# Kernel optimization log

Measured on AMD Instinct MI355X. Metric: run time of the kernel, lower is better.

Reference implementation:

```python
import jax, jax.numpy as jnp
import numpy as np

N_HEADS = 8
EMBED_DIM = 512
HEAD_DIM = EMBED_DIM // N_HEADS
INPUT_DIM = 512


def setup_inputs() -> dict:
    key = jax.random.key(0)
    ks = jax.random.split(key, 9)
    B, N = 4, 2048
    s_in = 1.0 / np.sqrt(INPUT_DIM)
    s_e = 1.0 / np.sqrt(EMBED_DIM)
    return {
        "q": jax.random.normal(ks[0], (B, N, INPUT_DIM), dtype=jnp.float32),
        "wq": jax.random.uniform(ks[1], (EMBED_DIM, INPUT_DIM), jnp.float32, -s_in, s_in),
        "bq": jax.random.uniform(ks[2], (EMBED_DIM,), jnp.float32, -s_in, s_in),
        "wk": jax.random.uniform(ks[3], (EMBED_DIM, INPUT_DIM), jnp.float32, -s_in, s_in),
        "bk": jax.random.uniform(ks[4], (EMBED_DIM,), jnp.float32, -s_in, s_in),
        "wv": jax.random.uniform(ks[5], (EMBED_DIM, INPUT_DIM), jnp.float32, -s_in, s_in),
        "bv": jax.random.uniform(ks[6], (EMBED_DIM,), jnp.float32, -s_in, s_in),
        "wo": jax.random.uniform(ks[7], (EMBED_DIM, EMBED_DIM), jnp.float32, -s_e, s_e),
        "bo": jax.random.uniform(ks[8], (EMBED_DIM,), jnp.float32, -s_e, s_e),
    }


def reference(q, wq, bq, wk, bk, wv, bv, wo, bo):
    B, N, _ = q.shape
    # linear projections (torch Linear: x @ W.T + b)
    Q = (q @ wq.T + bq).reshape(B, N, N_HEADS, HEAD_DIM).transpose(0, 2, 1, 3)
    K = (q @ wk.T + bk).reshape(B, N, N_HEADS, HEAD_DIM).transpose(0, 2, 1, 3)
    V = (q @ wv.T + bv).reshape(B, N, N_HEADS, HEAD_DIM).transpose(0, 2, 1, 3)
    scores = jnp.einsum("bhqd,bhkd->bhqk", Q, K) / jnp.sqrt(
        jnp.asarray(HEAD_DIM, dtype=q.dtype)
    )
    weights = jax.nn.softmax(scores, axis=-1)
    out = jnp.einsum("bhqk,bhkd->bhqd", weights, V)  # [B,H,N,Dh]
    out = out.transpose(0, 2, 1, 3).reshape(B, N, EMBED_DIM)
    return out @ wo.T + bo
```

## Files before the change

### kernel.cpp

```cpp
#include <hip/hip_runtime.h>
#include <hip/hip_bf16.h>
#include <math.h>

#define SEQ    2048
#define DH     64
#define EMB    512
#define INDIM  512
#define NHEADS 8
#define BATCH  4
#define MTOT   (BATCH * SEQ)

typedef __attribute__((ext_vector_type(8))) short bf16x8;
typedef __attribute__((ext_vector_type(4))) float f32x4;

__device__ __forceinline__ ushort f2bf(float x) {
  union { float f; unsigned u; } v; v.f = x;
  unsigned r = v.u + 0x7FFFu + ((v.u >> 16) & 1u);
  return (ushort)(r >> 16);
}

__device__ __forceinline__ unsigned cvt_pk_bf16(float lo, float hi) {
  unsigned r;
  asm("v_cvt_pk_bf16_f32 %0, %1, %2" : "=v"(r) : "v"(lo), "v"(hi));
  return r;
}

__device__ __forceinline__ float fast_exp2(float x) {
  float r;
  asm("v_exp_f32 %0, %1" : "=v"(r) : "v"(x));
  return r;
}

__device__ __forceinline__ void permswap32(unsigned &x, unsigned &y) {
  asm("v_permlane32_swap_b32 %0, %1" : "+v"(x), "+v"(y));
}

__global__ __launch_bounds__(256) void conv_bf16(const float* __restrict__ src,
                                                 ushort* __restrict__ dst, int n8) {
  const int i = blockIdx.x * 256 + threadIdx.x;
  if (i >= n8) return;
  const float4 a = ((const float4*)src)[i * 2];
  const float4 b = ((const float4*)src)[i * 2 + 1];
  uint4 o;
  o.x = cvt_pk_bf16(a.x, a.y);
  o.y = cvt_pk_bf16(a.z, a.w);
  o.z = cvt_pk_bf16(b.x, b.y);
  o.w = cvt_pk_bf16(b.z, b.w);
  ((uint4*)dst)[i] = o;
}

__global__ __launch_bounds__(256) void conv_bf16_w4(
    const float* __restrict__ w0, const float* __restrict__ w1,
    const float* __restrict__ w2, const float* __restrict__ w3,
    ushort* __restrict__ dst, int n8per) {
  const int i = blockIdx.x * 256 + threadIdx.x;
  if (i >= n8per) return;
  const float* src = (blockIdx.y == 0) ? w0 : (blockIdx.y == 1) ? w1
                   : (blockIdx.y == 2) ? w2 : w3;
  ushort* d = dst + (size_t)blockIdx.y * n8per * 8;
  const float4 a = ((const float4*)src)[i * 2];
  const float4 b = ((const float4*)src)[i * 2 + 1];
  uint4 o;
  o.x = cvt_pk_bf16(a.x, a.y);
  o.y = cvt_pk_bf16(a.z, a.w);
  o.z = cvt_pk_bf16(b.x, b.y);
  o.w = cvt_pk_bf16(b.z, b.w);
  ((uint4*)d)[i] = o;
}

template <int MODE>
__global__ __launch_bounds__(256) void mfma_gemm(
    const ushort* __restrict__ A, const ushort* __restrict__ W,
    const float* __restrict__ b0, const float* __restrict__ b1,
    const float* __restrict__ b2,
    ushort* __restrict__ outQ, ushort* __restrict__ outK,
    ushort* __restrict__ outVT, float* __restrict__ outF) {
  constexpr int BM = (MODE == 0) ? 128 : 64;
  constexpr int MF = (MODE == 0) ? 4 : 2;
  __shared__ __align__(16) char smem[MODE == 0 ? 35840 : 12288];
  ushort* As = (ushort*)smem;
  ushort* Bs = (ushort*)(smem + (MODE == 0 ? 8192 : 4096));
  ushort* Tl = (ushort*)smem;
  ushort* Tl2 = (ushort*)smem;

  const int bm = blockIdx.x * BM;
  const int bn = blockIdx.y * 128;
  const int tid = threadIdx.x;
  const int wave = tid >> 6, lane = tid & 63;
  const int g = lane >> 4, ln = lane & 15;
  const int wr = wave >> 1, wc = wave & 1;

  f32x4 acc[MF][4];
#pragma unroll
  for (int m = 0; m < MF; ++m)
#pragma unroll
    for (int n = 0; n < 4; ++n) acc[m][n] = (f32x4){0.f, 0.f, 0.f, 0.f};

  const size_t a_base = (size_t)(bm + wave * 16 + (lane >> 2)) * INDIM + (lane & 3) * 8;
  const size_t b_base = (size_t)(bn + wave * 16 + (lane >> 2)) * INDIM + (lane & 3) * 8;
  ushort* ldsA0 = As + wave * 512;
  ushort* ldsA1 = As + 2048 + wave * 512;
  ushort* ldsB0 = Bs + wave * 512;
  ushort* ldsB1 = Bs + 2048 + wave * 512;

  for (int k0 = 0; k0 < INDIM; k0 += 32) {
    __syncthreads();
    __builtin_amdgcn_global_load_lds(
        (const __attribute__((address_space(1))) void*)(A + a_base + k0),
        (__attribute__((address_space(3))) void*)ldsA0, 16, 0, 0);
    if (MODE == 0)
      __builtin_amdgcn_global_load_lds(
          (const __attribute__((address_space(1))) void*)(A + a_base + 64 * INDIM + k0),
          (__attribute__((address_space(3))) void*)ldsA1, 16, 0, 0);
    __builtin_amdgcn_global_load_lds(
        (const __attribute__((address_space(1))) void*)(W + b_base + k0),
        (__attribute__((address_space(3))) void*)ldsB0, 16, 0, 0);
    __builtin_amdgcn_global_load_lds(
        (const __attribute__((address_space(1))) void*)(W + b_base + 64 * INDIM + k0),
        (__attribute__((address_space(3))) void*)ldsB1, 16, 0, 0);
    __syncthreads();

    bf16x8 af[MF], bfv[4];
#pragma unroll
    for (int m = 0; m < MF; ++m)
      af[m] = *(const bf16x8*)&As[((MODE == 0 ? 64 : 32) * wr + 16 * m + ln) * 32 + 8 * g];
#pragma unroll
    for (int n = 0; n < 4; ++n)
      bfv[n] = *(const bf16x8*)&Bs[(64 * wc + 16 * n + ln) * 32 + 8 * g];
#pragma unroll
    for (int m = 0; m < MF; ++m)
#pragma unroll
      for (int n = 0; n < 4; ++n)
        acc[m][n] = __builtin_amdgcn_mfma_f32_16x16x32_bf16(af[m], bfv[n], acc[m][n], 0, 0, 0);
  }

  if (MODE == 1) {
#pragma unroll
    for (int n = 0; n < 4; ++n) {
      const int e = bn + 64 * wc + 16 * n + ln;
      const float bv = b0[e];
#pragma unroll
      for (int m = 0; m < MF; ++m)
#pragma unroll
        for (int r = 0; r < 4; ++r) {
          const int row = bm + 32 * wr + 16 * m + 4 * g + r;
          outF[(size_t)row * EMB + e] = acc[m][n][r] + bv;
        }
    }
    return;
  }

  const int which = bn >> 9;
  const float* bias = (which == 0) ? b0 : (which == 1) ? b1 : b2;

  if (which < 2) {
    const float scl = (which == 0) ? 0.18033688f : 1.0f;
    ushort* dst = (which == 0) ? outQ : outK;
    __syncthreads();
#pragma unroll
    for (int n = 0; n < 4; ++n) {
      const int cl = 64 * wc + 16 * n + ln;
      const float bv = bias[(bn & 511) + cl];
#pragma unroll
      for (int m = 0; m < 4; ++m)
#pragma unroll
        for (int r = 0; r < 4; ++r) {
          const int rl = 64 * wr + 16 * m + 4 * g + r;
          Tl2[rl * 136 + cl] = f2bf((acc[m][n][r] + bv) * scl);
        }
    }
    __syncthreads();
#pragma unroll
    for (int j = 0; j < 8; ++j) {
      const int cid = j * 256 + tid;
      const int seg = cid >> 3;
      const int l8 = cid & 7;
      const int rl = seg >> 1, half = seg & 1;
      const int row = bm + rl;
      const int b = row >> 11, nn = row & (SEQ - 1);
      const int h = ((bn & 511) >> 6) + half;
      const bf16x8 v = *(const bf16x8*)&Tl2[rl * 136 + half * 64 + l8 * 8];
      *(bf16x8*)&dst[(((size_t)(b * NHEADS + h) * SEQ) + nn) * DH + l8 * 8] = v;
    }
  } else {
    __syncthreads();
#pragma unroll
    for (int n = 0; n < 4; ++n) {
      const int cl = 64 * wc + 16 * n + ln;
      const float bv = bias[(bn & 511) + cl];
#pragma unroll
      for (int m = 0; m < 4; ++m)
#pragma unroll
        for (int r = 0; r < 4; ++r) {
          const int rl = 64 * wr + 16 * m + 4 * g + r;
          Tl[cl * 140 + rl] = f2bf(acc[m][n][r] + bv);
        }
    }
    __syncthreads();
    const int c = tid >> 1;
    const int rh = (tid & 1) * 64;
    const int e = (bn & 511) + c;
    const int h = e >> 6, d = e & 63;
    const int b = bm >> 11;
    const int nn0 = (bm & (SEQ - 1)) + rh;
    ushort* drow = outVT + (((size_t)(b * NHEADS + h) * DH) + d) * SEQ + nn0;
#pragma unroll
    for (int j = 0; j < 8; ++j)
      *(bf16x8*)&drow[j * 8] = *(const bf16x8*)&Tl[c * 140 + rh + j * 8];
  }
}

__global__ __launch_bounds__(256) void attn_mfma(const ushort* __restrict__ Q,
                                                 const ushort* __restrict__ K,
                                                 const ushort* __restrict__ VT,
                                                 ushort* __restrict__ O) {
  __shared__ __align__(16) ushort Kl[2][128 * 72];
  __shared__ __align__(16) ushort Vl[2][64 * 136];

  const int tid = threadIdx.x;
  const int wave = tid >> 6, lane = tid & 63;
  const int g = lane >> 4, ln = lane & 15;

  const int orig = blockIdx.x;
  const int swz = (orig & 7) * 64 + (orig >> 3);
  const int bh = swz >> 4;
  const int qx = swz & 15;
  const int qbase = qx * 128 + wave * 32;

  const ushort* Qb = Q + ((size_t)bh * SEQ + qbase) * DH;
  const ushort* Kb = K + (size_t)bh * SEQ * DH;
  const ushort* Vb = VT + (size_t)bh * DH * SEQ;

  const bf16x8 qfA0 = *(const bf16x8*)&Qb[ln * DH + 8 * g];
  const bf16x8 qfA1 = *(const bf16x8*)&Qb[ln * DH + 32 + 8 * g];
  const bf16x8 qfB0 = *(const bf16x8*)&Qb[(16 + ln) * DH + 8 * g];
  const bf16x8 qfB1 = *(const bf16x8*)&Qb[(16 + ln) * DH + 32 + 8 * g];

  bf16x8 vones;
#pragma unroll
  for (int i = 0; i < 8; ++i) vones[i] = (short)0x3F80;

  f32x4 oaccA[4], oaccB[4];
  f32x4 oaccDA = (f32x4){0.f, 0.f, 0.f, 0.f};
  f32x4 oaccDB = (f32x4){0.f, 0.f, 0.f, 0.f};
#pragma unroll
  for (int t = 0; t < 4; ++t) {
    oaccA[t] = (f32x4){0.f, 0.f, 0.f, 0.f};
    oaccB[t] = (f32x4){0.f, 0.f, 0.f, 0.f};
  }

  const int skv = tid >> 3, sd = (tid & 7) * 8;
  const int dt = tid >> 2, kc = (tid & 3) * 8;
  int pr[4];
#pragma unroll
  for (int j = 0; j < 4; ++j) {
    const int row = skv + 32 * j;
    pr[j] = row ^ (((((row >> 2) ^ (row >> 3)) & 1)) * 12);
  }

  bf16x8 kv[4], vv[4];
#pragma unroll
  for (int j = 0; j < 4; ++j) {
    kv[j] = *(const bf16x8*)&Kb[(size_t)(skv + 32 * j) * DH + sd];
    vv[j] = *(const bf16x8*)&Vb[(size_t)dt * SEQ + kc + 32 * j];
  }
#pragma unroll
  for (int j = 0; j < 4; ++j) {
    *(bf16x8*)&Kl[0][pr[j] * 72 + sd] = kv[j];
    *(bf16x8*)&Vl[0][dt * 136 + kc + 32 * j] = vv[j];
  }
#pragma unroll
  for (int j = 0; j < 4; ++j) {
    kv[j] = *(const bf16x8*)&Kb[(size_t)(128 + skv + 32 * j) * DH + sd];
    vv[j] = *(const bf16x8*)&Vb[(size_t)dt * SEQ + 128 + kc + 32 * j];
  }
  asm volatile("s_waitcnt lgkmcnt(0)" ::: "memory");
  __builtin_amdgcn_s_barrier();

  for (int it = 0; it < 16; ++it) {
    const int cur = it & 1;
    const ushort* Kc = Kl[cur];
    const ushort* Vc = Vl[cur];

    if (it < 15) {
      ushort* Kn = Kl[cur ^ 1];
      ushort* Vn = Vl[cur ^ 1];
#pragma unroll
      for (int j = 0; j < 4; ++j) {
        *(bf16x8*)&Kn[pr[j] * 72 + sd] = kv[j];
        *(bf16x8*)&Vn[dt * 136 + kc + 32 * j] = vv[j];
      }
    }
    {
      const int nxt = (it + 2 < 16) ? (it + 2) * 128 : 15 * 128;
#pragma unroll
      for (int j = 0; j < 4; ++j) {
        kv[j] = *(const bf16x8*)&Kb[(size_t)(nxt + skv + 32 * j) * DH + sd];
        vv[j] = *(const bf16x8*)&Vb[(size_t)dt * SEQ + nxt + kc + 32 * j];
      }
    }

#pragma unroll
    for (int s = 0; s < 2; ++s) {
      bf16x8 ka[4][2], vb[2][4];
#pragma unroll
      for (int t = 0; t < 4; ++t) {
        ka[t][0] = *(const bf16x8*)&Kc[(64 * s + 16 * t + ln) * 72 + 8 * g];
        ka[t][1] = *(const bf16x8*)&Kc[(64 * s + 16 * t + ln) * 72 + 32 + 8 * g];
      }
#pragma unroll
      for (int c = 0; c < 2; ++c)
#pragma unroll
        for (int t = 0; t < 4; ++t)
          vb[c][t] = *(const bf16x8*)&Vc[(16 * t + ln) * 136 + 64 * s + 32 * c + 8 * g];

      f32x4 sA0 = (f32x4){0.f, 0.f, 0.f, 0.f};
      f32x4 sA1 = sA0, sA2 = sA0, sA3 = sA0;
      f32x4 sB0 = sA0, sB1 = sA0, sB2 = sA0, sB3 = sA0;
      __builtin_amdgcn_s_setprio(1);
      sA0 = __builtin_amdgcn_mfma_f32_16x16x32_bf16(ka[0][0], qfA0, sA0, 0, 0, 0);
      sB0 = __builtin_amdgcn_mfma_f32_16x16x32_bf16(ka[0][0], qfB0, sB0, 0, 0, 0);
      sA1 = __builtin_amdgcn_mfma_f32_16x16x32_bf16(ka[1][0], qfA0, sA1, 0, 0, 0);
      sB1 = __builtin_amdgcn_mfma_f32_16x16x32_bf16(ka[1][0], qfB0, sB1, 0, 0, 0);
      sA2 = __builtin_amdgcn_mfma_f32_16x16x32_bf16(ka[2][0], qfA0, sA2, 0, 0, 0);
      sB2 = __builtin_amdgcn_mfma_f32_16x16x32_bf16(ka[2][0], qfB0, sB2, 0, 0, 0);
      sA3 = __builtin_amdgcn_mfma_f32_16x16x32_bf16(ka[3][0], qfA0, sA3, 0, 0, 0);
      sB3 = __builtin_amdgcn_mfma_f32_16x16x32_bf16(ka[3][0], qfB0, sB3, 0, 0, 0);
      sA0 = __builtin_amdgcn_mfma_f32_16x16x32_bf16(ka[0][1], qfA1, sA0, 0, 0, 0);
      sB0 = __builtin_amdgcn_mfma_f32_16x16x32_bf16(ka[0][1], qfB1, sB0, 0, 0, 0);
      sA1 = __builtin_amdgcn_mfma_f32_16x16x32_bf16(ka[1][1], qfA1, sA1, 0, 0, 0);
      sB1 = __builtin_amdgcn_mfma_f32_16x16x32_bf16(ka[1][1], qfB1, sB1, 0, 0, 0);
      sA2 = __builtin_amdgcn_mfma_f32_16x16x32_bf16(ka[2][1], qfA1, sA2, 0, 0, 0);
      sB2 = __builtin_amdgcn_mfma_f32_16x16x32_bf16(ka[2][1], qfB1, sB2, 0, 0, 0);
      sA3 = __builtin_amdgcn_mfma_f32_16x16x32_bf16(ka[3][1], qfA1, sA3, 0, 0, 0);
      sB3 = __builtin_amdgcn_mfma_f32_16x16x32_bf16(ka[3][1], qfB1, sB3, 0, 0, 0);
      __builtin_amdgcn_s_setprio(0);

      float pA0[4], pA1[4], pA2[4], pA3[4];
      float pB0[4], pB1[4], pB2[4], pB3[4];
#pragma unroll
      for (int r = 0; r < 4; ++r) {
        pA0[r] = fast_exp2(sA0[r]);
        pA1[r] = fast_exp2(sA1[r]);
        pA2[r] = fast_exp2(sA2[r]);
        pA3[r] = fast_exp2(sA3[r]);
        pB0[r] = fast_exp2(sB0[r]);
        pB1[r] = fast_exp2(sB1[r]);
        pB2[r] = fast_exp2(sB2[r]);
        pB3[r] = fast_exp2(sB3[r]);
      }

      unsigned aa0 = cvt_pk_bf16(pA0[0], pA0[1]);
      unsigned aa2 = cvt_pk_bf16(pA1[0], pA1[1]);
      unsigned aa1 = cvt_pk_bf16(pA0[2], pA0[3]);
      unsigned aa3 = cvt_pk_bf16(pA1[2], pA1[3]);
      permswap32(aa0, aa2);
      permswap32(aa1, aa3);
      unsigned ab0 = cvt_pk_bf16(pA2[0], pA2[1]);
      unsigned ab2 = cvt_pk_bf16(pA3[0], pA3[1]);
      unsigned ab1 = cvt_pk_bf16(pA2[2], pA2[3]);
      unsigned ab3 = cvt_pk_bf16(pA3[2], pA3[3]);
      permswap32(ab0, ab2);
      permswap32(ab1, ab3);
      unsigned ba0 = cvt_pk_bf16(pB0[0], pB0[1]);
      unsigned ba2 = cvt_pk_bf16(pB1[0], pB1[1]);
      unsigned ba1 = cvt_pk_bf16(pB0[2], pB0[3]);
      unsigned ba3 = cvt_pk_bf16(pB1[2], pB1[3]);
      permswap32(ba0, ba2);
      permswap32(ba1, ba3);
      unsigned bb0 = cvt_pk_bf16(pB2[0], pB2[1]);
      unsigned bb2 = cvt_pk_bf16(pB3[0], pB3[1]);
      unsigned bb1 = cvt_pk_bf16(pB2[2], pB2[3]);
      unsigned bb3 = cvt_pk_bf16(pB3[2], pB3[3]);
      permswap32(bb0, bb2);
      permswap32(bb1, bb3);
      union { unsigned u[4]; bf16x8 v; } paA0, paA1, paB0, paB1;
      paA0.u[0] = aa0; paA0.u[1] = aa1; paA0.u[2] = aa2; paA0.u[3] = aa3;
      paA1.u[0] = ab0; paA1.u[1] = ab1; paA1.u[2] = ab2; paA1.u[3] = ab3;
      paB0.u[0] = ba0; paB0.u[1] = ba1; paB0.u[2] = ba2; paB0.u[3] = ba3;
      paB1.u[0] = bb0; paB1.u[1] = bb1; paB1.u[2] = bb2; paB1.u[3] = bb3;

      __builtin_amdgcn_s_setprio(1);
#pragma unroll
      for (int t = 0; t < 4; ++t) {
        oaccA[t] = __builtin_amdgcn_mfma_f32_16x16x32_bf16(paA0.v, vb[0][t], oaccA[t], 0, 0, 0);
        oaccB[t] = __builtin_amdgcn_mfma_f32_16x16x32_bf16(paB0.v, vb[0][t], oaccB[t], 0, 0, 0);
        oaccA[t] = __builtin_amdgcn_mfma_f32_16x16x32_bf16(paA1.v, vb[1][t], oaccA[t], 0, 0, 0);
        oaccB[t] = __builtin_amdgcn_mfma_f32_16x16x32_bf16(paB1.v, vb[1][t], oaccB[t], 0, 0, 0);
      }
      oaccDA = __builtin_amdgcn_mfma_f32_16x16x32_bf16(paA0.v, vones, oaccDA, 0, 0, 0);
      oaccDB = __builtin_amdgcn_mfma_f32_16x16x32_bf16(paB0.v, vones, oaccDB, 0, 0, 0);
      oaccDA = __builtin_amdgcn_mfma_f32_16x16x32_bf16(paA1.v, vones, oaccDA, 0, 0, 0);
      oaccDB = __builtin_amdgcn_mfma_f32_16x16x32_bf16(paB1.v, vones, oaccDB, 0, 0, 0);
      __builtin_amdgcn_s_setprio(0);
    }

    asm volatile("s_waitcnt lgkmcnt(0)" ::: "memory");
    __builtin_amdgcn_s_barrier();
  }

  const int b = bh >> 3, h = bh & 7;
#pragma unroll
  for (int r = 0; r < 4; ++r) {
    const float irA = 1.0f / oaccDA[r];
    const float irB = 1.0f / oaccDB[r];
    ushort* opA = O + ((size_t)(b * SEQ) + qbase + 4 * g + r) * EMB + h * 64;
    ushort* opB = O + ((size_t)(b * SEQ) + qbase + 16 + 4 * g + r) * EMB + h * 64;
#pragma unroll
    for (int t = 0; t < 4; ++t) {
      opA[16 * t + ln] = f2bf(oaccA[t][r] * irA);
      opB[16 * t + ln] = f2bf(oaccB[t][r] * irB);
    }
  }
}

extern "C" void kernel_launch(void* const* d_in, const int* in_sizes, int n_in,
                              void* d_out, int out_size, void* d_ws, size_t ws_size,
                              hipStream_t stream) {
  const float* q  = (const float*)d_in[0];
  const float* wq = (const float*)d_in[1];
  const float* bq = (const float*)d_in[2];
  const float* wk = (const float*)d_in[3];
  const float* bk = (const float*)d_in[4];
  const float* wv = (const float*)d_in[5];
  const float* bv = (const float*)d_in[6];
  const float* wo = (const float*)d_in[7];
  const float* bo = (const float*)d_in[8];
  float* out = (float*)d_out;

  const size_t XSZ = (size_t)MTOT * INDIM;
  const size_t WSZ = (size_t)EMB * INDIM;
  const size_t QSZ = (size_t)BATCH * NHEADS * SEQ * DH;
  ushort* wsX = (ushort*)d_ws;
  ushort* wsW = wsX + XSZ;
  ushort* wsQ = wsW + 4 * WSZ;
  ushort* wsK = wsQ + QSZ;
  ushort* wsVT = wsK + QSZ;
  ushort* wsA = wsVT + QSZ;

  const dim3 blk(256);

  conv_bf16<<<dim3(XSZ / 8 / 256), blk, 0, stream>>>(q, wsX, XSZ / 8);
  conv_bf16_w4<<<dim3(WSZ / 8 / 256, 4), blk, 0, stream>>>(wq, wk, wv, wo, wsW, WSZ / 8);

  mfma_gemm<0><<<dim3(MTOT / 128, 1536 / 128), blk, 0, stream>>>(
      wsX, wsW, bq, bk, bv, wsQ, wsK, wsVT, nullptr);

  attn_mfma<<<dim3(512), blk, 0, stream>>>(wsQ, wsK, wsVT, wsA);

  mfma_gemm<1><<<dim3(MTOT / 64, EMB / 128), blk, 0, stream>>>(
      wsA, wsW + 3 * WSZ, bo, nullptr, nullptr, nullptr, nullptr, nullptr, out);
}
```

Baseline: 98.89 us.

## Split attention KV range across two thread halves and merge partial accumulators

The attention kernel now runs 512 threads per block. Each 256-thread half processes one half of the key/value sequence (1024 keys) for the same 128 queries, using 64-key tiles per iteration. The halves merge their partial output and denominator accumulators through shared memory at the end. This is split-K inside a block, meant to double the waves in flight per block and raise latency hiding and occupancy with only 512 blocks. The cost is an extra LDS reduction, smaller tiles per barrier, and a launch-bound that may constrain registers. The merge is exact only because the softmax uses no running max, which the kernel already did before.

```diff
diff --git a/kernel.cpp b/kernel.cpp
--- a/kernel.cpp
+++ b/kernel.cpp
@@ -210,15 +210,17 @@
   }
 }
 
-__global__ __launch_bounds__(256) void attn_mfma(const ushort* __restrict__ Q,
-                                                 const ushort* __restrict__ K,
-                                                 const ushort* __restrict__ VT,
-                                                 ushort* __restrict__ O) {
-  __shared__ __align__(16) ushort Kl[2][128 * 72];
-  __shared__ __align__(16) ushort Vl[2][64 * 136];
+__global__ __launch_bounds__(512, 4) void attn_mfma(const ushort* __restrict__ Q,
+                                                    const ushort* __restrict__ K,
+                                                    const ushort* __restrict__ VT,
+                                                    ushort* __restrict__ O) {
+  __shared__ __align__(16) ushort Kl[2][2][64 * 72];
+  __shared__ __align__(16) ushort Vl[2][2][64 * 72];
 
   const int tid = threadIdx.x;
-  const int wave = tid >> 6, lane = tid & 63;
+  const int half = tid >> 8;
+  const int ltid = tid & 255;
+  const int wave = ltid >> 6, lane = ltid & 63;
   const int g = lane >> 4, ln = lane & 15;
 
   const int orig = blockIdx.x;
@@ -226,6 +228,7 @@
   const int bh = swz >> 4;
   const int qx = swz & 15;
   const int qbase = qx * 128 + wave * 32;
+  const int kvbase = half << 10;
 
   const ushort* Qb = Q + ((size_t)bh * SEQ + qbase) * DH;
   const ushort* Kb = K + (size_t)bh * SEQ * DH;
@@ -249,167 +252,179 @@
     oaccB[t] = (f32x4){0.f, 0.f, 0.f, 0.f};
   }
 
-  const int skv = tid >> 3, sd = (tid & 7) * 8;
-  const int dt = tid >> 2, kc = (tid & 3) * 8;
-  int pr[4];
-#pragma unroll
-  for (int j = 0; j < 4; ++j) {
-    const int row = skv + 32 * j;
-    pr[j] = row ^ (((((row >> 2) ^ (row >> 3)) & 1)) * 12);
-  }
-
-  bf16x8 kv[4], vv[4];
-#pragma unroll
-  for (int j = 0; j < 4; ++j) {
-    kv[j] = *(const bf16x8*)&Kb[(size_t)(skv + 32 * j) * DH + sd];
-    vv[j] = *(const bf16x8*)&Vb[(size_t)dt * SEQ + kc + 32 * j];
-  }
-#pragma unroll
-  for (int j = 0; j < 4; ++j) {
-    *(bf16x8*)&Kl[0][pr[j] * 72 + sd] = kv[j];
-    *(bf16x8*)&Vl[0][dt * 136 + kc + 32 * j] = vv[j];
-  }
-#pragma unroll
-  for (int j = 0; j < 4; ++j) {
-    kv[j] = *(const bf16x8*)&Kb[(size_t)(128 + skv + 32 * j) * DH + sd];
-    vv[j] = *(const bf16x8*)&Vb[(size_t)dt * SEQ + 128 + kc + 32 * j];
-  }
+  const int skv = ltid >> 3, sd = (ltid & 7) * 8;
+  const int dt = ltid >> 2, kc = (ltid & 3) * 8;
+  const int pr0 = skv ^ (((((skv >> 2) ^ (skv >> 3)) & 1)) * 12);
+  const int s32 = skv + 32;
+  const int pr1 = s32 ^ (((((s32 >> 2) ^ (s32 >> 3)) & 1)) * 12);
+
+  bf16x8 k0v = *(const bf16x8*)&Kb[(size_t)(kvbase + skv) * DH + sd];
+  bf16x8 k1v = *(const bf16x8*)&Kb[(size_t)(kvbase + 32 + skv) * DH + sd];
+  bf16x8 v0v = *(const bf16x8*)&Vb[(size_t)dt * SEQ + kvbase + kc];
+  bf16x8 v1v = *(const bf16x8*)&Vb[(size_t)dt * SEQ + kvbase + 32 + kc];
+  *(bf16x8*)&Kl[half][0][pr0 * 72 + sd] = k0v;
+  *(bf16x8*)&Kl[half][0][pr1 * 72 + sd] = k1v;
+  *(bf16x8*)&Vl[half][0][dt * 72 + kc] = v0v;
+  *(bf16x8*)&Vl[half][0][dt * 72 + 32 + kc] = v1v;
+  k0v = *(const bf16x8*)&Kb[(size_t)(kvbase + 64 + skv) * DH + sd];
+  k1v = *(const bf16x8*)&Kb[(size_t)(kvbase + 96 + skv) * DH + sd];
+  v0v = *(const bf16x8*)&Vb[(size_t)dt * SEQ + kvbase + 64 + kc];
+  v1v = *(const bf16x8*)&Vb[(size_t)dt * SEQ + kvbase + 96 + kc];
   asm volatile("s_waitcnt lgkmcnt(0)" ::: "memory");
   __builtin_amdgcn_s_barrier();
 
   for (int it = 0; it < 16; ++it) {
     const int cur = it & 1;
-    const ushort* Kc = Kl[cur];
-    const ushort* Vc = Vl[cur];
+    const ushort* Kc = Kl[half][cur];
+    const ushort* Vc = Vl[half][cur];
 
     if (it < 15) {
-      ushort* Kn = Kl[cur ^ 1];
-      ushort* Vn = Vl[cur ^ 1];
-#pragma unroll
-      for (int j = 0; j < 4; ++j) {
-        *(bf16x8*)&Kn[pr[j] * 72 + sd] = kv[j];
-        *(bf16x8*)&Vn[dt * 136 + kc + 32 * j] = vv[j];
-      }
+      ushort* Kn = Kl[half][cur ^ 1];
+      ushort* Vn = Vl[half][cur ^ 1];
+      *(bf16x8*)&Kn[pr0 * 72 + sd] = k0v;
+      *(bf16x8*)&Kn[pr1 * 72 + sd] = k1v;
+      *(bf16x8*)&Vn[dt * 72 + kc] = v0v;
+      *(bf16x8*)&Vn[dt * 72 + 32 + kc] = v1v;
     }
     {
-      const int nxt = (it + 2 < 16) ? (it + 2) * 128 : 15 * 128;
-#pragma unroll
-      for (int j = 0; j < 4; ++j) {
-        kv[j] = *(const bf16x8*)&Kb[(size_t)(nxt + skv + 32 * j) * DH + sd];
-        vv[j] = *(const bf16x8*)&Vb[(size_t)dt * SEQ + nxt + kc + 32 * j];
-      }
-    }
-
-#pragma unroll
-    for (int s = 0; s < 2; ++s) {
-      bf16x8 ka[4][2], vb[2][4];
-#pragma unroll
-      for (int t = 0; t < 4; ++t) {
-        ka[t][0] = *(const bf16x8*)&Kc[(64 * s + 16 * t + ln) * 72 + 8 * g];
-        ka[t][1] = *(const bf16x8*)&Kc[(64 * s + 16 * t + ln) * 72 + 32 + 8 * g];
-      }
-#pragma unroll
-      for (int c = 0; c < 2; ++c)
-#pragma unroll
-        for (int t = 0; t < 4; ++t)
-          vb[c][t] = *(const bf16x8*)&Vc[(16 * t + ln) * 136 + 64 * s + 32 * c + 8 * g];
-
-      f32x4 sA0 = (f32x4){0.f, 0.f, 0.f, 0.f};
-      f32x4 sA1 = sA0, sA2 = sA0, sA3 = sA0;
-      f32x4 sB0 = sA0, sB1 = sA0, sB2 = sA0, sB3 = sA0;
-      __builtin_amdgcn_s_setprio(1);
-      sA0 = __builtin_amdgcn_mfma_f32_16x16x32_bf16(ka[0][0], qfA0, sA0, 0, 0, 0);
-      sB0 = __builtin_amdgcn_mfma_f32_16x16x32_bf16(ka[0][0], qfB0, sB0, 0, 0, 0);
-      sA1 = __builtin_amdgcn_mfma_f32_16x16x32_bf16(ka[1][0], qfA0, sA1, 0, 0, 0);
-      sB1 = __builtin_amdgcn_mfma_f32_16x16x32_bf16(ka[1][0], qfB0, sB1, 0, 0, 0);
-      sA2 = __builtin_amdgcn_mfma_f32_16x16x32_bf16(ka[2][0], qfA0, sA2, 0, 0, 0);
-      sB2 = __builtin_amdgcn_mfma_f32_16x16x32_bf16(ka[2][0], qfB0, sB2, 0, 0, 0);
-      sA3 = __builtin_amdgcn_mfma_f32_16x16x32_bf16(ka[3][0], qfA0, sA3, 0, 0, 0);
-      sB3 = __builtin_amdgcn_mfma_f32_16x16x32_bf16(ka[3][0], qfB0, sB3, 0, 0, 0);
-      sA0 = __builtin_amdgcn_mfma_f32_16x16x32_bf16(ka[0][1], qfA1, sA0, 0, 0, 0);
-      sB0 = __builtin_amdgcn_mfma_f32_16x16x32_bf16(ka[0][1], qfB1, sB0, 0, 0, 0);
-      sA1 = __builtin_amdgcn_mfma_f32_16x16x32_bf16(ka[1][1], qfA1, sA1, 0, 0, 0);
-      sB1 = __builtin_amdgcn_mfma_f32_16x16x32_bf16(ka[1][1], qfB1, sB1, 0, 0, 0);
-      sA2 = __builtin_amdgcn_mfma_f32_16x16x32_bf16(ka[2][1], qfA1, sA2, 0, 0, 0);
-      sB2 = __builtin_amdgcn_mfma_f32_16x16x32_bf16(ka[2][1], qfB1, sB2, 0, 0, 0);
-      sA3 = __builtin_amdgcn_mfma_f32_16x16x32_bf16(ka[3][1], qfA1, sA3, 0, 0, 0);
-      sB3 = __builtin_amdgcn_mfma_f32_16x16x32_bf16(ka[3][1], qfB1, sB3, 0, 0, 0);
-      __builtin_amdgcn_s_setprio(0);
-
-      float pA0[4], pA1[4], pA2[4], pA3[4];
-      float pB0[4], pB1[4], pB2[4], pB3[4];
-#pragma unroll
-      for (int r = 0; r < 4; ++r) {
-        pA0[r] = fast_exp2(sA0[r]);
-        pA1[r] = fast_exp2(sA1[r]);
-        pA2[r] = fast_exp2(sA2[r]);
-        pA3[r] = fast_exp2(sA3[r]);
-        pB0[r] = fast_exp2(sB0[r]);
-        pB1[r] = fast_exp2(sB1[r]);
-        pB2[r] = fast_exp2(sB2[r]);
-        pB3[r] = fast_exp2(sB3[r]);
-      }
-
-      unsigned aa0 = cvt_pk_bf16(pA0[0], pA0[1]);
-      unsigned aa2 = cvt_pk_bf16(pA1[0], pA1[1]);
-      unsigned aa1 = cvt_pk_bf16(pA0[2], pA0[3]);
-      unsigned aa3 = cvt_pk_bf16(pA1[2], pA1[3]);
-      permswap32(aa0, aa2);
-      permswap32(aa1, aa3);
-      unsigned ab0 = cvt_pk_bf16(pA2[0], pA2[1]);
-      unsigned ab2 = cvt_pk_bf16(pA3[0], pA3[1]);
-      unsigned ab1 = cvt_pk_bf16(pA2[2], pA2[3]);
-      unsigned ab3 = cvt_pk_bf16(pA3[2], pA3[3]);
-      permswap32(ab0, ab2);
-      permswap32(ab1, ab3);
-      unsigned ba0 = cvt_pk_bf16(pB0[0], pB0[1]);
-      unsigned ba2 = cvt_pk_bf16(pB1[0], pB1[1]);
-      unsigned ba1 = cvt_pk_bf16(pB0[2], pB0[3]);
-      unsigned ba3 = cvt_pk_bf16(pB1[2], pB1[3]);
-      permswap32(ba0, ba2);
-      permswap32(ba1, ba3);
-      unsigned bb0 = cvt_pk_bf16(pB2[0], pB2[1]);
-      unsigned bb2 = cvt_pk_bf16(pB3[0], pB3[1]);
-      unsigned bb1 = cvt_pk_bf16(pB2[2], pB2[3]);
-      unsigned bb3 = cvt_pk_bf16(pB3[2], pB3[3]);
-      permswap32(bb0, bb2);
-      permswap32(bb1, bb3);
-      union { unsigned u[4]; bf16x8 v; } paA0, paA1, paB0, paB1;
-      paA0.u[0] = aa0; paA0.u[1] = aa1; paA0.u[2] = aa2; paA0.u[3] = aa3;
-      paA1.u[0] = ab0; paA1.u[1] = ab1; paA1.u[2] = ab2; paA1.u[3] = ab3;
-      paB0.u[0] = ba0; paB0.u[1] = ba1; paB0.u[2] = ba2; paB0.u[3] = ba3;
-      paB1.u[0] = bb0; paB1.u[1] = bb1; paB1.u[2] = bb2; paB1.u[3] = bb3;
-
-      __builtin_amdgcn_s_setprio(1);
-#pragma unroll
-      for (int t = 0; t < 4; ++t) {
-        oaccA[t] = __builtin_amdgcn_mfma_f32_16x16x32_bf16(paA0.v, vb[0][t], oaccA[t], 0, 0, 0);
-        oaccB[t] = __builtin_amdgcn_mfma_f32_16x16x32_bf16(paB0.v, vb[0][t], oaccB[t], 0, 0, 0);
-        oaccA[t] = __builtin_amdgcn_mfma_f32_16x16x32_bf16(paA1.v, vb[1][t], oaccA[t], 0, 0, 0);
-        oaccB[t] = __builtin_amdgcn_mfma_f32_16x16x32_bf16(paB1.v, vb[1][t], oaccB[t], 0, 0, 0);
-      }
-      oaccDA = __builtin_amdgcn_mfma_f32_16x16x32_bf16(paA0.v, vones, oaccDA, 0, 0, 0);
-      oaccDB = __builtin_amdgcn_mfma_f32_16x16x32_bf16(paB0.v, vones, oaccDB, 0, 0, 0);
-      oaccDA = __builtin_amdgcn_mfma_f32_16x16x32_bf16(paA1.v, vones, oaccDA, 0, 0, 0);
-      oaccDB = __builtin_amdgcn_mfma_f32_16x16x32_bf16(paB1.v, vones, oaccDB, 0, 0, 0);
-      __builtin_amdgcn_s_setprio(0);
-    }
+      const int nxt = kvbase + ((it + 2 < 16) ? (it + 2) * 64 : 15 * 64);
+      k0v = *(const bf16x8*)&Kb[(size_t)(nxt + skv) * DH + sd];
+      k1v = *(const bf16x8*)&Kb[(size_t)(nxt + 32 + skv) * DH + sd];
+      v0v = *(const bf16x8*)&Vb[(size_t)dt * SEQ + nxt + kc];
+      v1v = *(const bf16x8*)&Vb[(size_t)dt * SEQ + nxt + 32 + kc];
+    }
+
+    bf16x8 ka[4][2], vb[2][4];
+#pragma unroll
+    for (int t = 0; t < 4; ++t) {
+      ka[t][0] = *(const bf16x8*)&Kc[(16 * t + ln) * 72 + 8 * g];
+      ka[t][1] = *(const bf16x8*)&Kc[(16 * t + ln) * 72 + 32 + 8 * g];
+    }
+#pragma unroll
+    for (int c = 0; c < 2; ++c)
+#pragma unroll
+      for (int t = 0; t < 4; ++t)
+        vb[c][t] = *(const bf16x8*)&Vc[(16 * t + ln) * 72 + 32 * c + 8 * g];
+
+    f32x4 sA0 = (f32x4){0.f, 0.f, 0.f, 0.f};
+    f32x4 sA1 = sA0, sA2 = sA0, sA3 = sA0;
+    f32x4 sB0 = sA0, sB1 = sA0, sB2 = sA0, sB3 = sA0;
+    __builtin_amdgcn_s_setprio(1);
+    sA0 = __builtin_amdgcn_mfma_f32_16x16x32_bf16(ka[0][0], qfA0, sA0, 0, 0, 0);
+    sB0 = __builtin_amdgcn_mfma_f32_16x16x32_bf16(ka[0][0], qfB0, sB0, 0, 0, 0);
+    sA1 = __builtin_amdgcn_mfma_f32_16x16x32_bf16(ka[1][0], qfA0, sA1, 0, 0, 0);
+    sB1 = __builtin_amdgcn_mfma_f32_16x16x32_bf16(ka[1][0], qfB0, sB1, 0, 0, 0);
+    sA2 = __builtin_amdgcn_mfma_f32_16x16x32_bf16(ka[2][0], qfA0, sA2, 0, 0, 0);
+    sB2 = __builtin_amdgcn_mfma_f32_16x16x32_bf16(ka[2][0], qfB0, sB2, 0, 0, 0);
+    sA3 = __builtin_amdgcn_mfma_f32_16x16x32_bf16(ka[3][0], qfA0, sA3, 0, 0, 0);
+    sB3 = __builtin_amdgcn_mfma_f32_16x16x32_bf16(ka[3][0], qfB0, sB3, 0, 0, 0);
+    sA0 = __builtin_amdgcn_mfma_f32_16x16x32_bf16(ka[0][1], qfA1, sA0, 0, 0, 0);
+    sB0 = __builtin_amdgcn_mfma_f32_16x16x32_bf16(ka[0][1], qfB1, sB0, 0, 0, 0);
+    sA1 = __builtin_amdgcn_mfma_f32_16x16x32_bf16(ka[1][1], qfA1, sA1, 0, 0, 0);
+    sB1 = __builtin_amdgcn_mfma_f32_16x16x32_bf16(ka[1][1], qfB1, sB1, 0, 0, 0);
+    sA2 = __builtin_amdgcn_mfma_f32_16x16x32_bf16(ka[2][1], qfA1, sA2, 0, 0, 0);
+    sB2 = __builtin_amdgcn_mfma_f32_16x16x32_bf16(ka[2][1], qfB1, sB2, 0, 0, 0);
+    sA3 = __builtin_amdgcn_mfma_f32_16x16x32_bf16(ka[3][1], qfA1, sA3, 0, 0, 0);
+    sB3 = __builtin_amdgcn_mfma_f32_16x16x32_bf16(ka[3][1], qfB1, sB3, 0, 0, 0);
+    __builtin_amdgcn_s_setprio(0);
+
+    float pA0[4], pA1[4], pA2[4], pA3[4];
+    float pB0[4], pB1[4], pB2[4], pB3[4];
+#pragma unroll
+    for (int r = 0; r < 4; ++r) {
+      pA0[r] = fast_exp2(sA0[r]);
+      pA1[r] = fast_exp2(sA1[r]);
+      pA2[r] = fast_exp2(sA2[r]);
+      pA3[r] = fast_exp2(sA3[r]);
+      pB0[r] = fast_exp2(sB0[r]);
+      pB1[r] = fast_exp2(sB1[r]);
+      pB2[r] = fast_exp2(sB2[r]);
+      pB3[r] = fast_exp2(sB3[r]);
+    }
+
+    unsigned aa0 = cvt_pk_bf16(pA0[0], pA0[1]);
+    unsigned aa2 = cvt_pk_bf16(pA1[0], pA1[1]);
+    unsigned aa1 = cvt_pk_bf16(pA0[2], pA0[3]);
+    unsigned aa3 = cvt_pk_bf16(pA1[2], pA1[3]);
+    permswap32(aa0, aa2);
+    permswap32(aa1, aa3);
+    unsigned ab0 = cvt_pk_bf16(pA2[0], pA2[1]);
+    unsigned ab2 = cvt_pk_bf16(pA3[0], pA3[1]);
+    unsigned ab1 = cvt_pk_bf16(pA2[2], pA2[3]);
+    unsigned ab3 = cvt_pk_bf16(pA3[2], pA3[3]);
+    permswap32(ab0, ab2);
+    permswap32(ab1, ab3);
+    unsigned ba0 = cvt_pk_bf16(pB0[0], pB0[1]);
+    unsigned ba2 = cvt_pk_bf16(pB1[0], pB1[1]);
+    unsigned ba1 = cvt_pk_bf16(pB0[2], pB0[3]);
+    unsigned ba3 = cvt_pk_bf16(pB1[2], pB1[3]);
+    permswap32(ba0, ba2);
+    permswap32(ba1, ba3);
+    unsigned bb0 = cvt_pk_bf16(pB2[0], pB2[1]);
+    unsigned bb2 = cvt_pk_bf16(pB3[0], pB3[1]);
+    unsigned bb1 = cvt_pk_bf16(pB2[2], pB2[3]);
+    unsigned bb3 = cvt_pk_bf16(pB3[2], pB3[3]);
+    permswap32(bb0, bb2);
+    permswap32(bb1, bb3);
+    union { unsigned u[4]; bf16x8 v; } paA0, paA1, paB0, paB1;
+    paA0.u[0] = aa0; paA0.u[1] = aa1; paA0.u[2] = aa2; paA0.u[3] = aa3;
+    paA1.u[0] = ab0; paA1.u[1] = ab1; paA1.u[2] = ab2; paA1.u[3] = ab3;
+    paB0.u[0] = ba0; paB0.u[1] = ba1; paB0.u[2] = ba2; paB0.u[3] = ba3;
+    paB1.u[0] = bb0; paB1.u[1] = bb1; paB1.u[2] = bb2; paB1.u[3] = bb3;
+
+    __builtin_amdgcn_s_setprio(1);
+#pragma unroll
+    for (int t = 0; t < 4; ++t) {
+      oaccA[t] = __builtin_amdgcn_mfma_f32_16x16x32_bf16(paA0.v, vb[0][t], oaccA[t], 0, 0, 0);
+      oaccB[t] = __builtin_amdgcn_mfma_f32_16x16x32_bf16(paB0.v, vb[0][t], oaccB[t], 0, 0, 0);
+      oaccA[t] = __builtin_amdgcn_mfma_f32_16x16x32_bf16(paA1.v, vb[1][t], oaccA[t], 0, 0, 0);
+      oaccB[t] = __builtin_amdgcn_mfma_f32_16x16x32_bf16(paB1.v, vb[1][t], oaccB[t], 0, 0, 0);
+    }
+    oaccDA = __builtin_amdgcn_mfma_f32_16x16x32_bf16(paA0.v, vones, oaccDA, 0, 0, 0);
+    oaccDB = __builtin_amdgcn_mfma_f32_16x16x32_bf16(paB0.v, vones, oaccDB, 0, 0, 0);
+    oaccDA = __builtin_amdgcn_mfma_f32_16x16x32_bf16(paA1.v, vones, oaccDA, 0, 0, 0);
+    oaccDB = __builtin_amdgcn_mfma_f32_16x16x32_bf16(paB1.v, vones, oaccDB, 0, 0, 0);
+    __builtin_amdgcn_s_setprio(0);
 
     asm volatile("s_waitcnt lgkmcnt(0)" ::: "memory");
     __builtin_amdgcn_s_barrier();
   }
 
-  const int b = bh >> 3, h = bh & 7;
-#pragma unroll
-  for (int r = 0; r < 4; ++r) {
-    const float irA = 1.0f / oaccDA[r];
-    const float irB = 1.0f / oaccDB[r];
-    ushort* opA = O + ((size_t)(b * SEQ) + qbase + 4 * g + r) * EMB + h * 64;
-    ushort* opB = O + ((size_t)(b * SEQ) + qbase + 16 + 4 * g + r) * EMB + h * 64;
-#pragma unroll
-    for (int t = 0; t < 4; ++t) {
-      opA[16 * t + ln] = f2bf(oaccA[t][r] * irA);
-      opB[16 * t + ln] = f2bf(oaccB[t][r] * irB);
+  float* Acc = (float*)&Kl[0][0][0];
+  float* Dl  = (float*)&Vl[0][0][0];
+  __syncthreads();
+  if (half == 0) {
+#pragma unroll
+    for (int t = 0; t < 4; ++t)
+#pragma unroll
+      for (int r = 0; r < 4; ++r) {
+        Acc[(wave * 32 + 4 * g + r) * 68 + 16 * t + ln] = oaccA[t][r];
+        Acc[(wave * 32 + 16 + 4 * g + r) * 68 + 16 * t + ln] = oaccB[t][r];
+      }
+    if (ln == 0) {
+#pragma unroll
+      for (int r = 0; r < 4; ++r) {
+        Dl[wave * 32 + 4 * g + r] = oaccDA[r];
+        Dl[wave * 32 + 16 + 4 * g + r] = oaccDB[r];
+      }
+    }
+  }
+  __syncthreads();
+  if (half == 1) {
+    const int b = bh >> 3, h = bh & 7;
+#pragma unroll
+    for (int r = 0; r < 4; ++r) {
+      const int rowA = wave * 32 + 4 * g + r;
+      const int rowB = rowA + 16;
+      const float irA = 1.0f / (Dl[rowA] + oaccDA[r]);
+      const float irB = 1.0f / (Dl[rowB] + oaccDB[r]);
+      ushort* opA = O + ((size_t)(b * SEQ) + qx * 128 + rowA) * EMB + h * 64;
+      ushort* opB = O + ((size_t)(b * SEQ) + qx * 128 + rowB) * EMB + h * 64;
+#pragma unroll
+      for (int t = 0; t < 4; ++t) {
+        opA[16 * t + ln] = f2bf((Acc[rowA * 68 + 16 * t + ln] + oaccA[t][r]) * irA);
+        opB[16 * t + ln] = f2bf((Acc[rowB * 68 + 16 * t + ln] + oaccB[t][r]) * irB);
+      }
     }
   }
 }
@@ -446,7 +461,7 @@
   mfma_gemm<0><<<dim3(MTOT / 128, 1536 / 128), blk, 0, stream>>>(
       wsX, wsW, bq, bk, bv, wsQ, wsK, wsVT, nullptr);
 
-  attn_mfma<<<dim3(512), blk, 0, stream>>>(wsQ, wsK, wsVT, wsA);
+  attn_mfma<<<dim3(512), dim3(512), 0, stream>>>(wsQ, wsK, wsVT, wsA);
 
   mfma_gemm<1><<<dim3(MTOT / 64, EMB / 128), blk, 0, stream>>>(
       wsA, wsW + 3 * WSZ, bo, nullptr, nullptr, nullptr, nullptr, nullptr, out);
```

After: 247.4 us. 2.5x slower.
